# Performance work log

Hardware: AMD Instinct MI355X
Metric: run time of the kernel (lower is better)

## Reference

```python
import jax, jax.numpy as jnp
import numpy as np
import math

N_HEADS = 12


def setup_inputs() -> dict:
    key = jax.random.key(0)
    ks = jax.random.split(key, 6)
    B, S, DIM = 4, 2048, 768
    h = jax.random.normal(ks[0], (B, S, DIM), dtype=jnp.float32)
    attn_mask = jnp.ones((B, 1, 1, S), dtype=jnp.int32)
    scale = 1.0 / math.sqrt(DIM)
    wq = jax.random.normal(ks[1], (DIM, DIM), dtype=jnp.float32) * scale
    wk = jax.random.normal(ks[2], (DIM, DIM), dtype=jnp.float32) * scale
    wv = jax.random.normal(ks[3], (DIM, DIM), dtype=jnp.float32) * scale
    wo = jax.random.normal(ks[4], (DIM, DIM), dtype=jnp.float32) * scale
    return {"h": h, "attn_mask": attn_mask, "wq": wq, "wk": wk, "wv": wv, "wo": wo}


def reference(h, attn_mask, wq, wk, wv, wo):
    B, S, dim = h.shape
    H = N_HEADS
    D = dim // H
    qk_scale = 1.0 / math.sqrt(D)
    # NOTE: original uses .view(B, H, S, D) on the [B, S, H*D] projection —
    # a raw reshape, NOT the usual (B,S,H,D)->(B,H,S,D) transpose. Reproduce exactly.
    hq = (h @ wq.T).reshape(B, H, S, D)
    hk = (h @ wk.T).reshape(B, H, S, D)
    hv = (h @ wv.T).reshape(B, H, S, D)
    scores = jnp.einsum("bhqd,bhkd->bhqk", hq, hk) * qk_scale  # [B,H,S,S]
    scores = jnp.where(attn_mask == 0, -jnp.inf, scores)
    attn = jax.nn.softmax(scores.astype(jnp.float32), axis=-1)
    ctx = jnp.einsum("bhqk,bhkd->bhqd", attn, hv)  # [B,H,S,D]
    # dropout is identity in eval mode
    ctx = ctx.reshape(B, S, H * D)
    return ctx @ wo.T
```

## Files before the change

### kernel.cpp

```cpp
#include <hip/hip_runtime.h>
#include <math.h>

typedef __bf16 bf16x8 __attribute__((ext_vector_type(8)));
typedef float  f32x4  __attribute__((ext_vector_type(4)));
typedef float  f32x16 __attribute__((ext_vector_type(16)));

#define MFMA16(a, b, c) __builtin_amdgcn_mfma_f32_16x16x32_bf16((a), (b), (c), 0, 0, 0)
#define MFMA32(a, b, c) __builtin_amdgcn_mfma_f32_32x32x16_bf16((a), (b), (c), 0, 0, 0)

__device__ __forceinline__ unsigned short f2bf(float f) {
    unsigned int u = __float_as_uint(f);
    u += 0x7fffu + ((u >> 16) & 1u);
    return (unsigned short)(u >> 16);
}

__device__ __forceinline__ void gll16(const unsigned short* g, unsigned short* l) {
    __builtin_amdgcn_global_load_lds(
        (const __attribute__((address_space(1))) unsigned int*)g,
        (__attribute__((address_space(3))) unsigned int*)l, 16, 0, 0);
}

__global__ __launch_bounds__(256) void convert_kernel(
    const float* __restrict__ h, const float* __restrict__ wq,
    const float* __restrict__ wk, const float* __restrict__ wv,
    const float* __restrict__ wo,
    unsigned short* __restrict__ hb, unsigned short* __restrict__ wb)
{
    const int NH4 = 1572864;
    const int NW4 = 147456;
    int i4 = blockIdx.x * 256 + threadIdx.x;
    const float4* src;
    unsigned short* dst;
    int off;
    float sc = 1.0f;
    if (i4 < NH4) {
        src = (const float4*)h; dst = hb; off = i4;
    } else {
        int j = i4 - NH4;
        int w = j / NW4;
        off = j - w * NW4;
        const float* s = (w == 0) ? wq : (w == 1) ? wk : (w == 2) ? wv : wo;
        if (w == 0) sc = 0.18033688011112042f;
        src = (const float4*)s;
        dst = wb + w * 589824;
    }
    float4 v = src[off];
    ushort4 o;
    o.x = f2bf(v.x * sc); o.y = f2bf(v.y * sc);
    o.z = f2bf(v.z * sc); o.w = f2bf(v.w * sc);
    ((ushort4*)dst)[off] = o;
}

template <typename OutT, int BM>
__global__ __launch_bounds__(256) void gemm_bt(
    const unsigned short* __restrict__ A,
    const unsigned short* __restrict__ Bm,
    OutT* __restrict__ C)
{
    constexpr int K = 768, N = 768;
    constexpr int MI = BM / 32;
    constexpr int NDMA = (BM == 128) ? 4 : 3;
    __shared__ unsigned short As[3][BM * 32];
    __shared__ unsigned short Bs[3][128 * 32];

    const int nwg  = gridDim.x;
    const int orig = blockIdx.x;
    const int lid  = (orig & 7) * (nwg >> 3) + (orig >> 3);
    const int ncol = (nwg * BM) >> 13;
    const int cix  = lid % ncol;
    const int bm   = (lid / ncol) * BM;
    const int nx   = cix % 6;
    const int bz   = cix / 6;
    const int bn   = nx * 128;

    const unsigned short* Bz = Bm + (size_t)bz * N * K;
    OutT* Cz = C + (size_t)bz * 8192 * N;

    const int tid  = threadIdx.x;
    const int wave = tid >> 6, lane = tid & 63;
    const int wm   = (wave & 1) * (BM / 2), wn = (wave >> 1) * 64;
    const int l16  = lane & 15, quad = lane >> 4;

    const int sr  = tid >> 2;
    const int sp8 = ((tid & 3) ^ (sr & 3)) * 8;
    const int slot8 = (quad ^ (l16 & 3)) * 8;

    auto stage = [&](int k0, int bi) {
        gll16(A  + (size_t)(bm + sr) * K      + k0 + sp8, As[bi] + tid * 8);
        if (BM == 128)
            gll16(A + (size_t)(bm + 64 + sr) * K + k0 + sp8, As[bi] + 2048 + tid * 8);
        gll16(Bz + (size_t)(bn + sr) * K      + k0 + sp8, Bs[bi] + tid * 8);
        gll16(Bz + (size_t)(bn + 64 + sr) * K + k0 + sp8, Bs[bi] + 2048 + tid * 8);
    };

    f32x4 acc[MI][4] = {};

    stage(0, 0);
    stage(32, 1);

    int cur = 0;
    for (int i = 0; i < 24; i++) {
        if (i < 23) {
            if (BM == 128) asm volatile("s_waitcnt vmcnt(4)\n\ts_barrier" ::: "memory");
            else           asm volatile("s_waitcnt vmcnt(3)\n\ts_barrier" ::: "memory");
        } else {
            asm volatile("s_waitcnt vmcnt(0)\n\ts_barrier" ::: "memory");
        }
        __builtin_amdgcn_sched_barrier(0);

        if (i < 22) {
            int nb = cur + 2; if (nb >= 3) nb -= 3;
            stage((i + 2) * 32, nb);
        }

        bf16x8 af[MI], bfv[4];
        #pragma unroll
        for (int ii = 0; ii < MI; ii++)
            af[ii] = *(const bf16x8*)(As[cur] + (wm + ii * 16 + l16) * 32 + slot8);
        #pragma unroll
        for (int jj = 0; jj < 4; jj++)
            bfv[jj] = *(const bf16x8*)(Bs[cur] + (wn + jj * 16 + l16) * 32 + slot8);
        #pragma unroll
        for (int ii = 0; ii < MI; ii++)
            #pragma unroll
            for (int jj = 0; jj < 4; jj++)
                acc[ii][jj] = MFMA16(af[ii], bfv[jj], acc[ii][jj]);

        cur = (cur == 2) ? 0 : cur + 1;
    }

    #pragma unroll
    for (int ii = 0; ii < MI; ii++) {
        #pragma unroll
        for (int jj = 0; jj < 4; jj++) {
            int row0 = bm + wm + ii * 16 + quad * 4;
            int col  = bn + wn + jj * 16 + l16;
            #pragma unroll
            for (int r = 0; r < 4; r++) {
                float v = acc[ii][jj][r];
                size_t idx = (size_t)(row0 + r) * N + col;
                if constexpr (sizeof(OutT) == 2) Cz[idx] = f2bf(v);
                else                             Cz[idx] = v;
            }
        }
    }
}

__global__ __launch_bounds__(256) void vtrans_kernel(
    const unsigned short* __restrict__ Vg,
    unsigned short* __restrict__ vt)
{
    constexpr int LDT = 72;
    __shared__ unsigned short Ts[64 * LDT];
    const int b = blockIdx.z, hh = blockIdx.y, kp0 = blockIdx.x * 64;
    const int tid = threadIdx.x;
    const size_t boff = (size_t)b * (24576 * 64);
    const int rowV0 = hh * 2048 + kp0;

    #pragma unroll
    for (int rep = 0; rep < 2; rep++) {
        int idx = rep * 256 + tid;
        int r = idx >> 3, dp = (idx & 7) * 8;
        uint4 v = *(const uint4*)(Vg + boff + (size_t)(rowV0 + r) * 64 + dp);
        unsigned short tmp[8];
        *(uint4*)tmp = v;
        #pragma unroll
        for (int i = 0; i < 8; i++) Ts[(dp + i) * LDT + r] = tmp[i];
    }
    __syncthreads();
    unsigned short* vtb = vt + ((size_t)(b * 12 + hh)) * 64 * 2048;
    #pragma unroll
    for (int rep = 0; rep < 2; rep++) {
        int idx = rep * 256 + tid;
        int d = idx >> 3, kp = (idx & 7) * 8;
        uint4 v = *(const uint4*)(Ts + d * LDT + kp);
        *(uint4*)(vtb + (size_t)d * 2048 + kp0 + kp) = v;
    }
}

__global__ __launch_bounds__(256) void attn_kernel(
    const unsigned short* __restrict__ Qg,
    const unsigned short* __restrict__ Kg,
    const unsigned short* __restrict__ vt,
    const int* __restrict__ mask,
    unsigned short* __restrict__ Og)
{
    __shared__ unsigned short Ks[6 * 2048];
    __shared__ unsigned short Vs[6 * 2048];
    __shared__ unsigned long long msh[32];

    const int orig = blockIdx.x;
    const int lid  = (orig & 7) * 96 + (orig >> 3);
    const int qt   = lid & 15;
    const int bh   = lid >> 4;
    const int hh   = bh % 12;
    const int b    = bh / 12;

    const int tid  = threadIdx.x;
    const int wave = tid >> 6, lane = tid & 63;
    const int c31  = lane & 31, h = lane >> 5;
    const size_t boff = (size_t)b * (24576 * 64);
    const int rowQ0 = hh * 2048 + qt * 128;
    const int rowK0 = hh * 2048;
    const unsigned short* vtg = vt + ((size_t)(b * 12 + hh)) * 64 * 2048;
    const int swk = (c31 & 7) ^ (c31 >> 3);
    const int swv = (c31 & 3) ^ ((c31 >> 2) & 3);

    const int srowK = tid >> 3;
    const int schK  = ((tid & 7) ^ (srowK & 7) ^ ((srowK >> 3) & 3)) * 8;
    const int srowV = tid >> 2;
    const int schV  = ((tid & 3) ^ (srowV & 3) ^ ((srowV >> 2) & 3)) * 8;

    auto stageKV = [&](int kt, int bi) {
        gll16(Kg  + boff + (size_t)(rowK0 + kt * 32 + srowK) * 64 + schK,
              Ks + bi * 2048 + tid * 8);
        gll16(vtg + (size_t)srowV * 2048 + kt * 32 + schV,
              Vs + bi * 2048 + tid * 8);
    };

    bf16x8 qf[4];
    {
        const unsigned short* qrow =
            Qg + boff + (size_t)(rowQ0 + wave * 32 + c31) * 64;
        #pragma unroll
        for (int c = 0; c < 4; c++)
            qf[c] = *(const bf16x8*)(qrow + (2 * c + h) * 8);
    }

    {
        const int4 a = *(const int4*)(mask + b * 2048 + tid * 8);
        const int4 c = *(const int4*)(mask + b * 2048 + tid * 8 + 4);
        unsigned char byte =
            (a.x != 0 ? 1u : 0u)       | (a.y != 0 ? 2u : 0u) |
            (a.z != 0 ? 4u : 0u)       | (a.w != 0 ? 8u : 0u) |
            (c.x != 0 ? 16u : 0u)      | (c.y != 0 ? 32u : 0u) |
            (c.z != 0 ? 64u : 0u)      | (c.w != 0 ? 128u : 0u);
        ((unsigned char*)msh)[tid] = byte;
    }
    __syncthreads();

    stageKV(0, 0);
    stageKV(1, 1);
    stageKV(2, 2);
    stageKV(3, 3);

    f32x16 acc[2] = {};
    f32x16 acc_l  = {};
    bf16x8 onesf;
    #pragma unroll
    for (int i = 0; i < 8; i++) onesf[i] = (__bf16)1.0f;

    int cur = 0;
    for (int j = 0; j < 32; j++) {
        if (j < 31) asm volatile("s_waitcnt vmcnt(4)\n\ts_barrier" ::: "memory");
        else        asm volatile("s_waitcnt vmcnt(0)\n\ts_barrier" ::: "memory");
        __builtin_amdgcn_sched_barrier(0);

        if (j < 30) {
            int nb0 = cur + 4; if (nb0 >= 6) nb0 -= 6;
            int nb1 = cur + 5; if (nb1 >= 6) nb1 -= 6;
            stageKV(2 * j + 4, nb0);
            stageKV(2 * j + 5, nb1);
        }

        const int c1 = (cur == 5) ? 0 : cur + 1;
        const unsigned int am0 = ((const unsigned int*)msh)[2 * j];
        const unsigned int am1 = ((const unsigned int*)msh)[2 * j + 1];
        const unsigned short* Kc0 = Ks + cur * 2048;
        const unsigned short* Vc0 = Vs + cur * 2048;
        const unsigned short* Kc1 = Ks + c1 * 2048;
        const unsigned short* Vc1 = Vs + c1 * 2048;
        const bool full = (am0 & am1) == 0xFFFFFFFFu;

        unsigned int a01[4], a23[4];
        {
            f32x16 z2 = {};
            __builtin_amdgcn_s_setprio(1);
            #pragma unroll
            for (int c = 0; c < 4; c++) {
                int ch = (2 * c + h) ^ swk;
                bf16x8 kf = *(const bf16x8*)(Kc0 + c31 * 64 + ch * 8);
                z2 = MFMA32(kf, qf[c], z2);
            }
            __builtin_amdgcn_s_setprio(0);
            if (full) {
                #pragma unroll
                for (int s = 0; s < 4; s++) {
                    float e0 = __builtin_amdgcn_exp2f(z2[4*s+0]);
                    float e1 = __builtin_amdgcn_exp2f(z2[4*s+1]);
                    float e2 = __builtin_amdgcn_exp2f(z2[4*s+2]);
                    float e3 = __builtin_amdgcn_exp2f(z2[4*s+3]);
                    asm("v_cvt_pk_bf16_f32 %0, %1, %2"
                        : "=v"(a01[s]) : "v"(e0), "v"(e1));
                    asm("v_cvt_pk_bf16_f32 %0, %1, %2"
                        : "=v"(a23[s]) : "v"(e2), "v"(e3));
                }
            } else {
                #pragma unroll
                for (int s = 0; s < 4; s++) {
                    unsigned int nib = (am0 >> (8 * s + 4 * h)) & 0xFu;
                    float e0 = __builtin_amdgcn_exp2f(z2[4*s+0]);
                    float e1 = __builtin_amdgcn_exp2f(z2[4*s+1]);
                    float e2 = __builtin_amdgcn_exp2f(z2[4*s+2]);
                    float e3 = __builtin_amdgcn_exp2f(z2[4*s+3]);
                    e0 = (nib & 1u) ? e0 : 0.f;
                    e1 = (nib & 2u) ? e1 : 0.f;
                    e2 = (nib & 4u) ? e2 : 0.f;
                    e3 = (nib & 8u) ? e3 : 0.f;
                    asm("v_cvt_pk_bf16_f32 %0, %1, %2"
                        : "=v"(a01[s]) : "v"(e0), "v"(e1));
                    asm("v_cvt_pk_bf16_f32 %0, %1, %2"
                        : "=v"(a23[s]) : "v"(e2), "v"(e3));
                }
            }
        }

        unsigned int b01[4], b23[4];
        {
            f32x16 z2 = {};
            __builtin_amdgcn_s_setprio(1);
            #pragma unroll
            for (int c = 0; c < 4; c++) {
                int ch = (2 * c + h) ^ swk;
                bf16x8 kf = *(const bf16x8*)(Kc1 + c31 * 64 + ch * 8);
                z2 = MFMA32(kf, qf[c], z2);
            }
            __builtin_amdgcn_s_setprio(0);
            if (full) {
                #pragma unroll
                for (int s = 0; s < 4; s++) {
                    float e0 = __builtin_amdgcn_exp2f(z2[4*s+0]);
                    float e1 = __builtin_amdgcn_exp2f(z2[4*s+1]);
                    float e2 = __builtin_amdgcn_exp2f(z2[4*s+2]);
                    float e3 = __builtin_amdgcn_exp2f(z2[4*s+3]);
                    asm("v_cvt_pk_bf16_f32 %0, %1, %2"
                        : "=v"(b01[s]) : "v"(e0), "v"(e1));
                    asm("v_cvt_pk_bf16_f32 %0, %1, %2"
                        : "=v"(b23[s]) : "v"(e2), "v"(e3));
                }
            } else {
                #pragma unroll
                for (int s = 0; s < 4; s++) {
                    unsigned int nib = (am1 >> (8 * s + 4 * h)) & 0xFu;
                    float e0 = __builtin_amdgcn_exp2f(z2[4*s+0]);
                    float e1 = __builtin_amdgcn_exp2f(z2[4*s+1]);
                    float e2 = __builtin_amdgcn_exp2f(z2[4*s+2]);
                    float e3 = __builtin_amdgcn_exp2f(z2[4*s+3]);
                    e0 = (nib & 1u) ? e0 : 0.f;
                    e1 = (nib & 2u) ? e1 : 0.f;
                    e2 = (nib & 4u) ? e2 : 0.f;
                    e3 = (nib & 8u) ? e3 : 0.f;
                    asm("v_cvt_pk_bf16_f32 %0, %1, %2"
                        : "=v"(b01[s]) : "v"(e0), "v"(e1));
                    asm("v_cvt_pk_bf16_f32 %0, %1, %2"
                        : "=v"(b23[s]) : "v"(e2), "v"(e3));
                }
            }
        }

        __builtin_amdgcn_s_setprio(1);
        #pragma unroll
        for (int kc = 0; kc < 2; kc++) {
            unsigned int x01 = a01[2 * kc], y01 = a01[2 * kc + 1];
            unsigned int x23 = a23[2 * kc], y23 = a23[2 * kc + 1];
            asm("v_permlane32_swap_b32 %0, %1" : "+v"(x01), "+v"(y01));
            asm("v_permlane32_swap_b32 %0, %1" : "+v"(x23), "+v"(y23));
            uint4 pfu;
            pfu.x = x01; pfu.y = x23; pfu.z = y01; pfu.w = y23;
            bf16x8 pf;
            __builtin_memcpy(&pf, &pfu, 16);
            #pragma unroll
            for (int nt = 0; nt < 2; nt++) {
                int chv = (2 * kc + h) ^ swv;
                bf16x8 vf = *(const bf16x8*)(Vc0 + (nt * 32 + c31) * 32 + chv * 8);
                acc[nt] = MFMA32(pf, vf, acc[nt]);
            }
            acc_l = MFMA32(pf, onesf, acc_l);
        }
        #pragma unroll
        for (int kc = 0; kc < 2; kc++) {
            unsigned int x01 = b01[2 * kc], y01 = b01[2 * kc + 1];
            unsigned int x23 = b23[2 * kc], y23 = b23[2 * kc + 1];
            asm("v_permlane32_swap_b32 %0, %1" : "+v"(x01), "+v"(y01));
            asm("v_permlane32_swap_b32 %0, %1" : "+v"(x23), "+v"(y23));
            uint4 pfu;
            pfu.x = x01; pfu.y = x23; pfu.z = y01; pfu.w = y23;
            bf16x8 pf;
            __builtin_memcpy(&pf, &pfu, 16);
            #pragma unroll
            for (int nt = 0; nt < 2; nt++) {
                int chv = (2 * kc + h) ^ swv;
                bf16x8 vf = *(const bf16x8*)(Vc1 + (nt * 32 + c31) * 32 + chv * 8);
                acc[nt] = MFMA32(pf, vf, acc[nt]);
            }
            acc_l = MFMA32(pf, onesf, acc_l);
        }
        __builtin_amdgcn_s_setprio(0);

        cur = (cur >= 4) ? cur - 4 : cur + 2;
    }

    #pragma unroll
    for (int reg = 0; reg < 16; reg++) {
        int rowfn = (reg & 3) + 8 * (reg >> 2) + 4 * h;
        float li = __builtin_amdgcn_rcpf(acc_l[reg]);
        int row = rowQ0 + wave * 32 + rowfn;
        #pragma unroll
        for (int nt = 0; nt < 2; nt++)
            Og[boff + (size_t)row * 64 + nt * 32 + c31] = f2bf(acc[nt][reg] * li);
    }
}

extern "C" void kernel_launch(void* const* d_in, const int* in_sizes, int n_in,
                              void* d_out, int out_size, void* d_ws, size_t ws_size,
                              hipStream_t stream)
{
    const float* h    = (const float*)d_in[0];
    const int*   mask = (const int*)d_in[1];
    const float* wq   = (const float*)d_in[2];
    const float* wk   = (const float*)d_in[3];
    const float* wv   = (const float*)d_in[4];
    const float* wo   = (const float*)d_in[5];

    unsigned short* hb  = (unsigned short*)d_ws;
    unsigned short* wb  = hb + 6291456;
    unsigned short* qkv = wb + 4 * 589824;
    unsigned short* ctx = qkv + (size_t)3 * 6291456;

    convert_kernel<<<8448, 256, 0, stream>>>(h, wq, wk, wv, wo, hb, wb);
    gemm_bt<unsigned short, 128><<<1152, 256, 0, stream>>>(hb, wb, qkv);
    vtrans_kernel<<<dim3(32, 12, 4), 256, 0, stream>>>(
        qkv + (size_t)2 * 6291456, hb);
    attn_kernel<<<768, 256, 0, stream>>>(
        qkv, qkv + 6291456, hb, mask, ctx);
    gemm_bt<float, 64><<<768, 256, 0, stream>>>(
        ctx, wb + (size_t)3 * 589824, (float*)d_out);
}
```

Before: 229.1 us.

## Fuse V transpose into attention kernel via register-staged LDS scatter

Drops the separate vtrans kernel. The attention kernel now loads V rows from global memory into registers and scatter-writes them transposed into a swizzled LDS layout one stage ahead, while K keeps using direct global-to-LDS loads. This removes one kernel launch and a full write and re-read of the transposed V buffer. In exchange it adds per-element 2-byte LDS stores and register pressure inside the main loop, and changes the waitcnt/barrier pipeline accounting.

Result: slower. 246.5 us (+7.6%).

```diff
diff --git a/kernel.cpp b/kernel.cpp
--- a/kernel.cpp
+++ b/kernel.cpp
@@ -59,7 +59,6 @@
 {
     constexpr int K = 768, N = 768;
     constexpr int MI = BM / 32;
-    constexpr int NDMA = (BM == 128) ? 4 : 3;
     __shared__ unsigned short As[3][BM * 32];
     __shared__ unsigned short Bs[3][128 * 32];
 
@@ -146,42 +145,10 @@
     }
 }
 
-__global__ __launch_bounds__(256) void vtrans_kernel(
-    const unsigned short* __restrict__ Vg,
-    unsigned short* __restrict__ vt)
-{
-    constexpr int LDT = 72;
-    __shared__ unsigned short Ts[64 * LDT];
-    const int b = blockIdx.z, hh = blockIdx.y, kp0 = blockIdx.x * 64;
-    const int tid = threadIdx.x;
-    const size_t boff = (size_t)b * (24576 * 64);
-    const int rowV0 = hh * 2048 + kp0;
-
-    #pragma unroll
-    for (int rep = 0; rep < 2; rep++) {
-        int idx = rep * 256 + tid;
-        int r = idx >> 3, dp = (idx & 7) * 8;
-        uint4 v = *(const uint4*)(Vg + boff + (size_t)(rowV0 + r) * 64 + dp);
-        unsigned short tmp[8];
-        *(uint4*)tmp = v;
-        #pragma unroll
-        for (int i = 0; i < 8; i++) Ts[(dp + i) * LDT + r] = tmp[i];
-    }
-    __syncthreads();
-    unsigned short* vtb = vt + ((size_t)(b * 12 + hh)) * 64 * 2048;
-    #pragma unroll
-    for (int rep = 0; rep < 2; rep++) {
-        int idx = rep * 256 + tid;
-        int d = idx >> 3, kp = (idx & 7) * 8;
-        uint4 v = *(const uint4*)(Ts + d * LDT + kp);
-        *(uint4*)(vtb + (size_t)d * 2048 + kp0 + kp) = v;
-    }
-}
-
 __global__ __launch_bounds__(256) void attn_kernel(
     const unsigned short* __restrict__ Qg,
     const unsigned short* __restrict__ Kg,
-    const unsigned short* __restrict__ vt,
+    const unsigned short* __restrict__ Vg,
     const int* __restrict__ mask,
     unsigned short* __restrict__ Og)
 {
@@ -202,20 +169,34 @@
     const size_t boff = (size_t)b * (24576 * 64);
     const int rowQ0 = hh * 2048 + qt * 128;
     const int rowK0 = hh * 2048;
-    const unsigned short* vtg = vt + ((size_t)(b * 12 + hh)) * 64 * 2048;
     const int swk = (c31 & 7) ^ (c31 >> 3);
-    const int swv = (c31 & 3) ^ ((c31 >> 2) & 3);
 
     const int srowK = tid >> 3;
     const int schK  = ((tid & 7) ^ (srowK & 7) ^ ((srowK >> 3) & 3)) * 8;
-    const int srowV = tid >> 2;
-    const int schV  = ((tid & 3) ^ (srowV & 3) ^ ((srowV >> 2) & 3)) * 8;
-
-    auto stageKV = [&](int kt, int bi) {
-        gll16(Kg  + boff + (size_t)(rowK0 + kt * 32 + srowK) * 64 + schK,
+
+    auto stageK = [&](int kt, int bi) {
+        gll16(Kg + boff + (size_t)(rowK0 + kt * 32 + srowK) * 64 + schK,
               Ks + bi * 2048 + tid * 8);
-        gll16(vtg + (size_t)srowV * 2048 + kt * 32 + schV,
-              Vs + bi * 2048 + tid * 8);
+    };
+
+    const int vs_  = tid >> 3;
+    const int vd0  = (tid & 7) * 8;
+    auto loadV = [&](int kt) -> uint4 {
+        return *(const uint4*)(Vg + boff +
+                 (size_t)(rowK0 + kt * 32 + vs_) * 64 + vd0);
+    };
+    const int vc_  = vs_ >> 3;
+    const int vsl  = vs_ & 7;
+    auto writeV = [&](int bi, uint4 v) {
+        unsigned short tmp[8];
+        *(uint4*)tmp = v;
+        unsigned short* base = Vs + bi * 2048;
+        #pragma unroll
+        for (int i = 0; i < 8; i++) {
+            int d = vd0 + i;
+            int f = (d & 3) ^ ((d >> 2) & 3) ^ ((d >> 4) & 3);
+            base[d * 32 + ((vc_ ^ f) << 3) + vsl] = tmp[i];
+        }
     };
 
     bf16x8 qf[4];
@@ -239,10 +220,14 @@
     }
     __syncthreads();
 
-    stageKV(0, 0);
-    stageKV(1, 1);
-    stageKV(2, 2);
-    stageKV(3, 3);
+    uint4 va0 = loadV(0), va1 = loadV(1);
+    stageK(0, 0);
+    stageK(1, 1);
+    writeV(0, va0);
+    writeV(1, va1);
+    va0 = loadV(2); va1 = loadV(3);
+    stageK(2, 2);
+    stageK(3, 3);
 
     f32x16 acc[2] = {};
     f32x16 acc_l  = {};
@@ -252,16 +237,25 @@
 
     int cur = 0;
     for (int j = 0; j < 32; j++) {
-        if (j < 31) asm volatile("s_waitcnt vmcnt(4)\n\ts_barrier" ::: "memory");
-        else        asm volatile("s_waitcnt vmcnt(0)\n\ts_barrier" ::: "memory");
+        if (j < 31) asm volatile("s_waitcnt vmcnt(2) lgkmcnt(0)\n\ts_barrier" ::: "memory");
+        else        asm volatile("s_waitcnt vmcnt(0) lgkmcnt(0)\n\ts_barrier" ::: "memory");
         __builtin_amdgcn_sched_barrier(0);
 
+        if (j <= 30) {
+            int wb0 = cur + 2; if (wb0 >= 6) wb0 -= 6;
+            int wb1 = cur + 3; if (wb1 >= 6) wb1 -= 6;
+            writeV(wb0, va0);
+            writeV(wb1, va1);
+        }
         if (j < 30) {
             int nb0 = cur + 4; if (nb0 >= 6) nb0 -= 6;
             int nb1 = cur + 5; if (nb1 >= 6) nb1 -= 6;
-            stageKV(2 * j + 4, nb0);
-            stageKV(2 * j + 5, nb1);
-        }
+            va0 = loadV(2 * j + 4);
+            va1 = loadV(2 * j + 5);
+            stageK(2 * j + 4, nb0);
+            stageK(2 * j + 5, nb1);
+        }
+        __builtin_amdgcn_sched_barrier(0);
 
         const int c1 = (cur == 5) ? 0 : cur + 1;
         const unsigned int am0 = ((const unsigned int*)msh)[2 * j];
@@ -371,8 +365,10 @@
             __builtin_memcpy(&pf, &pfu, 16);
             #pragma unroll
             for (int nt = 0; nt < 2; nt++) {
-                int chv = (2 * kc + h) ^ swv;
-                bf16x8 vf = *(const bf16x8*)(Vc0 + (nt * 32 + c31) * 32 + chv * 8);
+                int d = nt * 32 + c31;
+                int fv = (d & 3) ^ ((d >> 2) & 3) ^ ((d >> 4) & 3);
+                int chv = (2 * kc + h) ^ fv;
+                bf16x8 vf = *(const bf16x8*)(Vc0 + d * 32 + chv * 8);
                 acc[nt] = MFMA32(pf, vf, acc[nt]);
             }
             acc_l = MFMA32(pf, onesf, acc_l);
@@ -389,8 +385,10 @@
             __builtin_memcpy(&pf, &pfu, 16);
             #pragma unroll
             for (int nt = 0; nt < 2; nt++) {
-                int chv = (2 * kc + h) ^ swv;
-                bf16x8 vf = *(const bf16x8*)(Vc1 + (nt * 32 + c31) * 32 + chv * 8);
+                int d = nt * 32 + c31;
+                int fv = (d & 3) ^ ((d >> 2) & 3) ^ ((d >> 4) & 3);
+                int chv = (2 * kc + h) ^ fv;
+                bf16x8 vf = *(const bf16x8*)(Vc1 + d * 32 + chv * 8);
                 acc[nt] = MFMA32(pf, vf, acc[nt]);
             }
             acc_l = MFMA32(pf, onesf, acc_l);
@@ -429,10 +427,8 @@
 
     convert_kernel<<<8448, 256, 0, stream>>>(h, wq, wk, wv, wo, hb, wb);
     gemm_bt<unsigned short, 128><<<1152, 256, 0, stream>>>(hb, wb, qkv);
-    vtrans_kernel<<<dim3(32, 12, 4), 256, 0, stream>>>(
-        qkv + (size_t)2 * 6291456, hb);
     attn_kernel<<<768, 256, 0, stream>>>(
-        qkv, qkv + 6291456, hb, mask, ctx);
+        qkv, qkv + 6291456, qkv + (size_t)2 * 6291456, mask, ctx);
     gemm_bt<float, 64><<<768, 256, 0, stream>>>(
         ctx, wb + (size_t)3 * 589824, (float*)d_out);
 }
```

## Switch projection GEMMs to 32x32 MFMA tiles with new LDS swizzle

Applied to the files above, without the earlier changes.

Rewrites the bf16 GEMM inner loop to use 32x32x16 MFMA instructions on 2x2 per-wave tiles instead of 16x16x32 on 4x4 tiles. It also changes the LDS swizzle so the new 32-row read pattern avoids bank conflicts. The output-projection GEMM moves from 64-row to 128-row blocks, halving its grid to 384 workgroups. The aim is fewer LDS reads per MFMA and higher matrix-core throughput, at the cost of less parallelism in the output GEMM and a strided epilogue store pattern.

New measurement: 226.0 us. No clear change (-1.4%).

```diff
diff --git a/kernel.cpp b/kernel.cpp
--- a/kernel.cpp
+++ b/kernel.cpp
@@ -51,24 +51,22 @@
     ((ushort4*)dst)[off] = o;
 }
 
-template <typename OutT, int BM>
+template <typename OutT>
 __global__ __launch_bounds__(256) void gemm_bt(
     const unsigned short* __restrict__ A,
     const unsigned short* __restrict__ Bm,
     OutT* __restrict__ C)
 {
     constexpr int K = 768, N = 768;
-    constexpr int MI = BM / 32;
-    constexpr int NDMA = (BM == 128) ? 4 : 3;
-    __shared__ unsigned short As[3][BM * 32];
+    __shared__ unsigned short As[3][128 * 32];
     __shared__ unsigned short Bs[3][128 * 32];
 
     const int nwg  = gridDim.x;
     const int orig = blockIdx.x;
     const int lid  = (orig & 7) * (nwg >> 3) + (orig >> 3);
-    const int ncol = (nwg * BM) >> 13;
+    const int ncol = nwg >> 6;
     const int cix  = lid % ncol;
-    const int bm   = (lid / ncol) * BM;
+    const int bm   = (lid / ncol) * 128;
     const int nx   = cix % 6;
     const int bz   = cix / 6;
     const int bn   = nx * 128;
@@ -78,34 +76,29 @@
 
     const int tid  = threadIdx.x;
     const int wave = tid >> 6, lane = tid & 63;
-    const int wm   = (wave & 1) * (BM / 2), wn = (wave >> 1) * 64;
-    const int l16  = lane & 15, quad = lane >> 4;
+    const int wm   = (wave & 1) * 64, wn = (wave >> 1) * 64;
+    const int c31  = lane & 31, h = lane >> 5;
 
     const int sr  = tid >> 2;
-    const int sp8 = ((tid & 3) ^ (sr & 3)) * 8;
-    const int slot8 = (quad ^ (l16 & 3)) * 8;
+    const int sp8 = ((tid & 3) ^ (sr & 3) ^ ((sr >> 2) & 3)) * 8;
+    const int swr = (c31 & 3) ^ ((c31 >> 2) & 3);
 
     auto stage = [&](int k0, int bi) {
         gll16(A  + (size_t)(bm + sr) * K      + k0 + sp8, As[bi] + tid * 8);
-        if (BM == 128)
-            gll16(A + (size_t)(bm + 64 + sr) * K + k0 + sp8, As[bi] + 2048 + tid * 8);
+        gll16(A  + (size_t)(bm + 64 + sr) * K + k0 + sp8, As[bi] + 2048 + tid * 8);
         gll16(Bz + (size_t)(bn + sr) * K      + k0 + sp8, Bs[bi] + tid * 8);
         gll16(Bz + (size_t)(bn + 64 + sr) * K + k0 + sp8, Bs[bi] + 2048 + tid * 8);
     };
 
-    f32x4 acc[MI][4] = {};
+    f32x16 acc[2][2] = {};
 
     stage(0, 0);
     stage(32, 1);
 
     int cur = 0;
     for (int i = 0; i < 24; i++) {
-        if (i < 23) {
-            if (BM == 128) asm volatile("s_waitcnt vmcnt(4)\n\ts_barrier" ::: "memory");
-            else           asm volatile("s_waitcnt vmcnt(3)\n\ts_barrier" ::: "memory");
-        } else {
-            asm volatile("s_waitcnt vmcnt(0)\n\ts_barrier" ::: "memory");
-        }
+        if (i < 23) asm volatile("s_waitcnt vmcnt(4)\n\ts_barrier" ::: "memory");
+        else        asm volatile("s_waitcnt vmcnt(0)\n\ts_barrier" ::: "memory");
         __builtin_amdgcn_sched_barrier(0);
 
         if (i < 22) {
@@ -113,37 +106,38 @@
             stage((i + 2) * 32, nb);
         }
 
-        bf16x8 af[MI], bfv[4];
-        #pragma unroll
-        for (int ii = 0; ii < MI; ii++)
-            af[ii] = *(const bf16x8*)(As[cur] + (wm + ii * 16 + l16) * 32 + slot8);
-        #pragma unroll
-        for (int jj = 0; jj < 4; jj++)
-            bfv[jj] = *(const bf16x8*)(Bs[cur] + (wn + jj * 16 + l16) * 32 + slot8);
-        #pragma unroll
-        for (int ii = 0; ii < MI; ii++)
-            #pragma unroll
-            for (int jj = 0; jj < 4; jj++)
-                acc[ii][jj] = MFMA16(af[ii], bfv[jj], acc[ii][jj]);
+        bf16x8 af[2][2], bfv[2][2];
+        #pragma unroll
+        for (int mi = 0; mi < 2; mi++)
+            #pragma unroll
+            for (int c = 0; c < 2; c++) {
+                int ch = (2 * c + h) ^ swr;
+                af[mi][c]  = *(const bf16x8*)(As[cur] + (wm + mi * 32 + c31) * 32 + ch * 8);
+                bfv[mi][c] = *(const bf16x8*)(Bs[cur] + (wn + mi * 32 + c31) * 32 + ch * 8);
+            }
+        #pragma unroll
+        for (int mi = 0; mi < 2; mi++)
+            #pragma unroll
+            for (int ni = 0; ni < 2; ni++)
+                #pragma unroll
+                for (int c = 0; c < 2; c++)
+                    acc[mi][ni] = MFMA32(af[mi][c], bfv[ni][c], acc[mi][ni]);
 
         cur = (cur == 2) ? 0 : cur + 1;
     }
 
     #pragma unroll
-    for (int ii = 0; ii < MI; ii++) {
-        #pragma unroll
-        for (int jj = 0; jj < 4; jj++) {
-            int row0 = bm + wm + ii * 16 + quad * 4;
-            int col  = bn + wn + jj * 16 + l16;
-            #pragma unroll
-            for (int r = 0; r < 4; r++) {
-                float v = acc[ii][jj][r];
-                size_t idx = (size_t)(row0 + r) * N + col;
-                if constexpr (sizeof(OutT) == 2) Cz[idx] = f2bf(v);
-                else                             Cz[idx] = v;
-            }
-        }
-    }
+    for (int mi = 0; mi < 2; mi++)
+        #pragma unroll
+        for (int ni = 0; ni < 2; ni++)
+            #pragma unroll
+            for (int reg = 0; reg < 16; reg++) {
+                int rowfn = (reg & 3) + 8 * (reg >> 2) + 4 * h;
+                size_t idx = (size_t)(bm + wm + mi * 32 + rowfn) * N
+                           + (bn + wn + ni * 32 + c31);
+                if constexpr (sizeof(OutT) == 2) Cz[idx] = f2bf(acc[mi][ni][reg]);
+                else                             Cz[idx] = acc[mi][ni][reg];
+            }
 }
 
 __global__ __launch_bounds__(256) void vtrans_kernel(
@@ -428,11 +422,11 @@
     unsigned short* ctx = qkv + (size_t)3 * 6291456;
 
     convert_kernel<<<8448, 256, 0, stream>>>(h, wq, wk, wv, wo, hb, wb);
-    gemm_bt<unsigned short, 128><<<1152, 256, 0, stream>>>(hb, wb, qkv);
+    gemm_bt<unsigned short><<<1152, 256, 0, stream>>>(hb, wb, qkv);
     vtrans_kernel<<<dim3(32, 12, 4), 256, 0, stream>>>(
         qkv + (size_t)2 * 6291456, hb);
     attn_kernel<<<768, 256, 0, stream>>>(
         qkv, qkv + 6291456, hb, mask, ctx);
-    gemm_bt<float, 64><<<768, 256, 0, stream>>>(
+    gemm_bt<float><<<384, 256, 0, stream>>>(
         ctx, wb + (size_t)3 * 589824, (float*)d_out);
 }
```
